# Kernel tuning notes

Measured on AMD Instinct MI355X. Metric: run time of the kernel, lower is better.

## Reference

```python
import jax, jax.numpy as jnp
import numpy as np
import math

N_ENT = 200000
N_USERS = 100000
N_FACTORS = 4
N_REL = 26
CH = 64
N_EDGES = 1000000
NNZ = 1000000
KG_HEADS = 2


def scatter_softmax(scores, seg, num_segments):
    # numerically-stable softmax over groups defined by seg (per-head softmax)
    m = jax.ops.segment_max(scores, seg, num_segments=num_segments)
    m = jnp.where(jnp.isfinite(m), m, 0.0)
    e = jnp.exp(scores - m[seg])
    d = jax.ops.segment_sum(e, seg, num_segments=num_segments)
    return e / d[seg]


def setup_inputs() -> dict:
    key = jax.random.key(0)
    ks = jax.random.split(key, 11)
    return {
        "entity_emb": jax.random.normal(ks[0], (N_ENT, CH), dtype=jnp.float32) * 0.1,
        "user_emb": jax.random.normal(ks[1], (N_USERS, CH), dtype=jnp.float32) * 0.1,
        "latent_emb": jax.random.normal(ks[2], (N_FACTORS, CH), dtype=jnp.float32) * 0.1,
        "edge_index": jax.random.randint(ks[3], (2, N_EDGES), 0, N_ENT),
        "edge_type": jax.random.randint(ks[4], (N_EDGES,), 1, N_REL),  # in [1, N_REL-1]
        "ui_rows": jax.random.randint(ks[5], (NNZ,), 0, N_USERS),
        "ui_cols": jax.random.randint(ks[6], (NNZ,), 0, N_ENT),
        "ui_vals": jax.random.uniform(ks[7], (NNZ,), dtype=jnp.float32),
        "weight": jax.random.normal(ks[8], (N_REL - 1, CH), dtype=jnp.float32) * 0.1,
        "disen_weight_att": jax.random.normal(ks[9], (N_FACTORS, N_REL - 1), dtype=jnp.float32) * 0.1,
        "kg_W_r": jax.random.normal(ks[10], (CH, CH), dtype=jnp.float32) * (1.0 / math.sqrt(CH)),
    }


def reference(entity_emb, user_emb, latent_emb, edge_index, edge_type,
              ui_rows, ui_cols, ui_vals, weight, disen_weight_att, kg_W_r):
    head, tail = edge_index[0], edge_index[1]
    d_k = CH // KG_HEADS

    # --- Invariant_Capture.relation_aware_att ---
    rel_emb = weight[edge_type - 1]            # [E, C] gather
    h_emb = entity_emb[head]                   # [E, C] gather
    q = (h_emb @ kg_W_r).reshape(-1, KG_HEADS, d_k)
    k = (rel_emb @ kg_W_r).reshape(-1, KG_HEADS, d_k)
    score_r = ((q * k).sum(-1) / math.sqrt(d_k)).mean(-1)   # [E]
    rel_attn = scatter_softmax(score_r, head, N_ENT)

    # --- Invariant_Capture.kg_inv_capture ---
    t_emb = entity_emb[tail]                   # [E, C] gather
    r_emb = rel_emb * rel_attn[:, None]
    # bmm(cat(h,r), cat(t,r)^T) == h.t + r.r per edge
    score_trip = (h_emb * t_emb).sum(-1) + (r_emb * r_emb).sum(-1)
    kg_mask = scatter_softmax(score_trip, head, N_ENT)       # invariant_mask [E]

    # --- Aggregator: KG scatter-mean with invariant mask ---
    neigh = t_emb * rel_emb * kg_mask[:, None]               # [E, C]
    sums = jax.ops.segment_sum(neigh, head, num_segments=N_ENT)
    cnt = jax.ops.segment_sum(jnp.ones((neigh.shape[0],), dtype=neigh.dtype), head, num_segments=N_ENT)
    entity_agg = sums / jnp.maximum(cnt, 1.0)[:, None]       # scatter_mean

    # --- Aggregator: user side ---
    score = jax.nn.softmax(user_emb @ latent_emb.T, axis=1)  # [U, F]
    user_agg = jax.ops.segment_sum(entity_emb[ui_cols] * ui_vals[:, None], ui_rows, num_segments=N_USERS)
    disen_weight = jax.nn.softmax(disen_weight_att, axis=-1) @ weight  # [F, C]
    # (expand(U,F,C) * score[:,:,None]).sum(1) == score @ disen_weight
    user_agg = user_agg * (score @ disen_weight) + user_agg

    return jnp.concatenate([entity_agg, user_agg], axis=0)   # [N_ENT+N_USERS, C]
```

## Files before the change

### kernel.cpp

```cpp
#include <hip/hip_runtime.h>
#include <math.h>

#define N_ENT 200000
#define N_USERS 100000
#define NKEY 300000
#define N_FACTORS 4
#define NREL1 25
#define CH 64
#define N_EDGES 1000000
#define NNZ 1000000
#define NREC 2000000
#define BSHIFT 11
#define BKEYS 2048
#define NBUCKET 147
#define TILE 2048
#define NBLK_FILL ((NREC + TILE - 1) / TILE)
#define CAP 32768
#define NCONVB ((N_ENT * 8 + 1023) / 1024)

#define SCORE_SCALE 0.08838834764831845f
#define INV_Q14 6.103888176768602e-05f

__device__ __forceinline__ float red8(float d) {
    d += __shfl_xor(d, 1);
    d += __shfl_xor(d, 2);
    d += __shfl_xor(d, 4);
    return d;
}
__device__ __forceinline__ float dot4(float4 a, float4 b) {
    return a.x * b.x + a.y * b.y + a.z * b.z + a.w * b.w;
}
__device__ __forceinline__ unsigned short f2bf(float f) {
    unsigned u = __float_as_uint(f);
    u += 0x7FFFu + ((u >> 16) & 1u);
    return (unsigned short)(u >> 16);
}
__device__ __forceinline__ float bf2f(unsigned short u) {
    return __uint_as_float(((unsigned)u) << 16);
}
__device__ __forceinline__ float4 bf4lo(uint4 t) {
    return make_float4(__uint_as_float(t.x << 16), __uint_as_float(t.x & 0xFFFF0000u),
                       __uint_as_float(t.y << 16), __uint_as_float(t.y & 0xFFFF0000u));
}
__device__ __forceinline__ float4 bf4hi(uint4 t) {
    return make_float4(__uint_as_float(t.z << 16), __uint_as_float(t.z & 0xFFFF0000u),
                       __uint_as_float(t.w << 16), __uint_as_float(t.w & 0xFFFF0000u));
}

__device__ __forceinline__
void precompute_dev(int tid, unsigned char* shmraw,
                    const float* __restrict__ W,
                    const float* __restrict__ weight,
                    const float* __restrict__ datt,
                    float* __restrict__ Mvec,
                    float* __restrict__ wnorm,
                    float* __restrict__ disen) {
    float* sW   = (float*)shmraw;
    float* sw   = sW + 4096;
    float* sWWt = sw + 1600;
    for (int i = tid; i < 64 * 64; i += 256) sW[i] = W[i];
    for (int i = tid; i < NREL1 * 64; i += 256) sw[i] = weight[i];
    __syncthreads();
    for (int e = tid; e < 64 * 64; e += 256) {
        int i = e >> 6, j = e & 63;
        float s = 0.f;
        for (int k = 0; k < 64; ++k) s += sW[i * 64 + k] * sW[j * 64 + k];
        sWWt[e] = s;
    }
    __syncthreads();
    for (int e = tid; e < NREL1 * 64; e += 256) {
        int r = e >> 6, i = e & 63;
        float s = 0.f;
        for (int j = 0; j < 64; ++j) s += sWWt[i * 64 + j] * sw[r * 64 + j];
        Mvec[e] = s;
    }
    for (int r = tid; r < NREL1; r += 256) {
        float s = 0.f;
        for (int j = 0; j < 64; ++j) { float v = sw[r * 64 + j]; s += v * v; }
        wnorm[r] = s;
    }
    for (int e = tid; e < N_FACTORS * 64; e += 256) {
        int f = e >> 6, c = e & 63;
        float m = -1e30f;
        for (int r = 0; r < NREL1; ++r) m = fmaxf(m, datt[f * NREL1 + r]);
        float ssum = 0.f, acc = 0.f;
        for (int r = 0; r < NREL1; ++r) {
            float p = expf(datt[f * NREL1 + r] - m);
            ssum += p;
            acc += p * sw[r * 64 + c];
        }
        disen[e] = acc / ssum;
    }
}

__global__ void binpre_k(const int* __restrict__ head, const int* __restrict__ tail,
                         const int* __restrict__ etype,
                         const int* __restrict__ rows, const int* __restrict__ cols,
                         const float* __restrict__ vals,
                         unsigned* __restrict__ gcur,
                         uint2* __restrict__ stg,
                         const float* __restrict__ W,
                         const float* __restrict__ weight,
                         const float* __restrict__ datt,
                         float* __restrict__ Mvec,
                         float* __restrict__ wnorm,
                         float* __restrict__ disen) {
    __shared__ __align__(16) unsigned char shmraw[39936];
    int tid = threadIdx.x;
    if (blockIdx.x >= NBLK_FILL) {
        precompute_dev(tid, shmraw, W, weight, datt, Mvec, wnorm, disen);
        return;
    }
    unsigned* hist  = (unsigned*)shmraw;
    unsigned* base  = hist + NBUCKET;
    unsigned* gbase = base + NBUCKET;
    unsigned* wsum  = gbase + NBUCKET;
    uint2*    lrec  = (uint2*)(shmraw + 2048);

    int tile0 = blockIdx.x * TILE;
    int tile_n = min(TILE, NREC - tile0);
    for (int b = tid; b < NBUCKET; b += 256) hist[b] = 0u;
    __syncthreads();
    unsigned key[8], pay[8], rank[8];
    for (int r = 0; r < 8; ++r) {
        int li = r * 256 + tid;
        key[r] = 0xFFFFFFFFu;
        if (li < tile_n) {
            int idx = tile0 + li;
            unsigned k, p;
            if (idx < N_EDGES) {
                k = (unsigned)head[idx];
                p = (unsigned)tail[idx] | ((unsigned)(etype[idx] - 1) << 18);
            } else {
                int j = idx - N_EDGES;
                k = (unsigned)(N_ENT + rows[j]);
                unsigned q = (unsigned)(vals[j] * 16383.f + 0.5f);
                p = (unsigned)cols[j] | (q << 18);
            }
            key[r] = k; pay[r] = p;
            rank[r] = atomicAdd(&hist[k >> BSHIFT], 1u);
        }
    }
    __syncthreads();
    unsigned h0 = (tid < NBUCKET) ? hist[tid] : 0u;
    unsigned v = h0;
    int lane = tid & 63, wid = tid >> 6;
    for (int o = 1; o < 64; o <<= 1) {
        unsigned t = __shfl_up(v, o);
        if (lane >= o) v += t;
    }
    if (lane == 63) wsum[wid] = v;
    __syncthreads();
    unsigned pre = 0;
    for (int w = 0; w < wid; ++w) pre += wsum[w];
    if (tid < NBUCKET) {
        base[tid] = pre + v - h0;
        gbase[tid] = (unsigned)tid * CAP + (h0 ? atomicAdd(&gcur[tid], h0) : 0u);
    }
    __syncthreads();
    for (int r = 0; r < 8; ++r) {
        if (key[r] != 0xFFFFFFFFu) {
            unsigned b = key[r] >> BSHIFT;
            lrec[base[b] + rank[r]] = make_uint2(key[r], pay[r]);
        }
    }
    __syncthreads();
    for (int i = tid; i < tile_n; i += 256) {
        uint2 rec = lrec[i];
        unsigned b = rec.x >> BSHIFT;
        unsigned dst = gbase[b] + ((unsigned)i - base[b]);
        if (dst < (b + 1u) * CAP) stg[dst] = rec;
    }
}

__device__ __forceinline__
void place_bucket_dev(int b, int tid, const uint2* __restrict__ stg,
                      const unsigned* __restrict__ gcur,
                      unsigned* __restrict__ offs, unsigned* __restrict__ csr,
                      unsigned* shm) {
    unsigned c = (tid < NBUCKET) ? gcur[tid] : 0u;
    if (c > CAP) c = CAP;
    if (tid < 256) shm[tid] = c;
    __syncthreads();
    for (int o = 1; o < 256; o <<= 1) {
        unsigned t = (tid >= o && tid < 256) ? shm[tid - o] : 0u;
        __syncthreads();
        if (tid < 256) shm[tid] += t;
        __syncthreads();
    }
    if (tid == 0) {
        unsigned cb = gcur[b]; if (cb > CAP) cb = CAP;
        shm[3073] = cb;
        shm[3072] = shm[b] - cb;
        if (b == NBUCKET - 1) offs[NKEY] = shm[NBUCKET - 1];
    }
    __syncthreads();
    unsigned n = shm[3073], gb = shm[3072];
    const uint2* seg = stg + (size_t)b * CAP;
    unsigned* cnt = shm;
    unsigned* sc  = shm + 2048;
    cnt[tid * 2] = 0u; cnt[tid * 2 + 1] = 0u;
    __syncthreads();
    for (unsigned i = tid; i < n; i += 1024) {
        unsigned kk = seg[i].x - ((unsigned)b << BSHIFT);
        atomicAdd(&cnt[kk], 1u);
    }
    __syncthreads();
    unsigned c0 = cnt[tid * 2], c1 = cnt[tid * 2 + 1];
    unsigned tsum = c0 + c1;
    sc[tid] = tsum; __syncthreads();
    for (int o = 1; o < 1024; o <<= 1) {
        unsigned t = (tid >= o) ? sc[tid - o] : 0u;
        __syncthreads();
        sc[tid] += t;
        __syncthreads();
    }
    unsigned e0 = sc[tid] - tsum;
    unsigned e1 = e0 + c0;
    int k0 = (b << BSHIFT) + tid * 2;
    if (k0 < NKEY)     offs[k0]     = gb + e0;
    if (k0 + 1 < NKEY) offs[k0 + 1] = gb + e1;
    cnt[tid * 2] = e0; cnt[tid * 2 + 1] = e1;
    __syncthreads();
    for (unsigned i = tid; i < n; i += 1024) {
        uint2 rec = seg[i];
        unsigned kk = rec.x - ((unsigned)b << BSHIFT);
        unsigned pos = atomicAdd(&cnt[kk], 1u);
        csr[gb + pos] = rec.y;
    }
}

__device__ __forceinline__
void convE_dev(int cb, int tid, const float* __restrict__ ent,
               const float* __restrict__ Mvec,
               uint4* __restrict__ entb, unsigned short* __restrict__ E16,
               unsigned* shm) {
    float4* sM = (float4*)shm;
    for (int i = tid; i < NREL1 * 16; i += 1024) sM[i] = ((const float4*)Mvec)[i];
    __syncthreads();
    int idx = cb * 1024 + tid;
    int h = idx >> 3;
    int sub = tid & 7;
    if (h >= N_ENT) return;
    const float4* e4 = (const float4*)ent;
    float4 a = e4[h * 16 + sub * 2], b4 = e4[h * 16 + sub * 2 + 1];
    uint4 o;
    o.x = (unsigned)f2bf(a.x)  | ((unsigned)f2bf(a.y)  << 16);
    o.y = (unsigned)f2bf(a.z)  | ((unsigned)f2bf(a.w)  << 16);
    o.z = (unsigned)f2bf(b4.x) | ((unsigned)f2bf(b4.y) << 16);
    o.w = (unsigned)f2bf(b4.z) | ((unsigned)f2bf(b4.w) << 16);
    entb[h * 8 + sub] = o;
    for (int r = 0; r < NREL1; ++r) {
        float d = dot4(a, sM[r * 16 + sub * 2]) + dot4(b4, sM[r * 16 + sub * 2 + 1]);
        d = red8(d);
        if (sub == (r & 7)) E16[h * NREL1 + r] = f2bf(__expf(d * SCORE_SCALE));
    }
}

__global__ void placeconv_k(const uint2* __restrict__ stg,
                            const unsigned* __restrict__ gcur,
                            unsigned* __restrict__ offs,
                            unsigned* __restrict__ csr,
                            const float* __restrict__ ent,
                            const float* __restrict__ Mvec,
                            uint4* __restrict__ entb,
                            unsigned short* __restrict__ E16) {
    __shared__ __align__(16) unsigned shm[3074];
    int b = blockIdx.x;
    if (b < NBUCKET)
        place_bucket_dev(b, threadIdx.x, stg, gcur, offs, csr, shm);
    else
        convE_dev(b - NBUCKET, threadIdx.x, ent, Mvec, entb, E16, shm);
}

__global__ void binplace3_k(const uint2* __restrict__ stg,
                            const unsigned* __restrict__ gcur,
                            unsigned* __restrict__ offs,
                            unsigned* __restrict__ csr) {
    __shared__ __align__(16) unsigned shm[3074];
    place_bucket_dev(blockIdx.x, threadIdx.x, stg, gcur, offs, csr, shm);
}

template<bool FAST>
__global__ void gather8_k(const float* __restrict__ ent,
                          const uint4* __restrict__ entb,
                          const unsigned short* __restrict__ E16,
                          const float* __restrict__ weight,
                          const float* __restrict__ Mvec,
                          const float* __restrict__ wnorm,
                          const float* __restrict__ uemb,
                          const float* __restrict__ lat,
                          const float* __restrict__ disen,
                          const unsigned* __restrict__ offs,
                          const unsigned* __restrict__ csr,
                          float* __restrict__ out) {
    int gid = blockIdx.x * 256 + threadIdx.x;
    int key = gid >> 3;
    int sub = threadIdx.x & 7;
    if (key >= NKEY) return;
    unsigned beg = offs[key], end = offs[key + 1];
    const float4* e4 = (const float4*)ent;
    const float4* w4 = (const float4*)weight;
    float4* o4 = (float4*)out;
    const float4 z = make_float4(0.f, 0.f, 0.f, 0.f);

    if (key < N_ENT) {
        int h = key;
        if (beg == end) {
            o4[h * 16 + sub * 2] = z;
            o4[h * 16 + sub * 2 + 1] = z;
            return;
        }
        float4 hv0, hv1;
        if (FAST) {
            uint4 hb = entb[h * 8 + sub];
            hv0 = bf4lo(hb); hv1 = bf4hi(hb);
        } else {
            hv0 = e4[h * 16 + sub * 2]; hv1 = e4[h * 16 + sub * 2 + 1];
        }
        float dr = 0.f;
        if (FAST) {
            for (unsigned i = beg + sub; i < end; i += 8)
                dr += bf2f(E16[h * NREL1 + (csr[i] >> 18)]);
            dr = red8(dr);
        } else {
            for (unsigned i = beg; i < end; ++i) {
                int r = csr[i] >> 18;
                float d = dot4(hv0, ((const float4*)Mvec)[r * 16 + sub * 2]) +
                          dot4(hv1, ((const float4*)Mvec)[r * 16 + sub * 2 + 1]);
                dr += __expf(red8(d) * SCORE_SCALE);
            }
        }
        float inv_dr = 1.0f / dr;
        float4 a0 = z, a1 = z;
        float dt = 0.f;
        unsigned i = beg;
        for (; i + 2 <= end; i += 2) {
            unsigned p0 = csr[i], p1 = csr[i + 1];
            int t0 = p0 & 0x3FFFF, r0 = p0 >> 18;
            int t1 = p1 & 0x3FFFF, r1 = p1 >> 18;
            float4 tv00, tv01, tv10, tv11;
            if (FAST) {
                uint4 tb0 = entb[t0 * 8 + sub];
                uint4 tb1 = entb[t1 * 8 + sub];
                tv00 = bf4lo(tb0); tv01 = bf4hi(tb0);
                tv10 = bf4lo(tb1); tv11 = bf4hi(tb1);
            } else {
                tv00 = e4[t0 * 16 + sub * 2]; tv01 = e4[t0 * 16 + sub * 2 + 1];
                tv10 = e4[t1 * 16 + sub * 2]; tv11 = e4[t1 * 16 + sub * 2 + 1];
            }
            float d0 = red8(dot4(hv0, tv00) + dot4(hv1, tv01));
            float d1 = red8(dot4(hv0, tv10) + dot4(hv1, tv11));
            float er0, er1;
            if (FAST) {
                er0 = bf2f(E16[h * NREL1 + r0]);
                er1 = bf2f(E16[h * NREL1 + r1]);
            } else {
                float q0 = dot4(hv0, ((const float4*)Mvec)[r0 * 16 + sub * 2]) +
                           dot4(hv1, ((const float4*)Mvec)[r0 * 16 + sub * 2 + 1]);
                float q1 = dot4(hv0, ((const float4*)Mvec)[r1 * 16 + sub * 2]) +
                           dot4(hv1, ((const float4*)Mvec)[r1 * 16 + sub * 2 + 1]);
                er0 = __expf(red8(q0) * SCORE_SCALE);
                er1 = __expf(red8(q1) * SCORE_SCALE);
            }
            float ra0 = er0 * inv_dr, ra1 = er1 * inv_dr;
            float et0 = __expf(d0 + ra0 * ra0 * wnorm[r0]);
            float et1 = __expf(d1 + ra1 * ra1 * wnorm[r1]);
            dt += et0 + et1;
            float4 wv;
            wv = w4[r0 * 16 + sub * 2];
            a0.x += et0 * tv00.x * wv.x; a0.y += et0 * tv00.y * wv.y;
            a0.z += et0 * tv00.z * wv.z; a0.w += et0 * tv00.w * wv.w;
            wv = w4[r0 * 16 + sub * 2 + 1];
            a1.x += et0 * tv01.x * wv.x; a1.y += et0 * tv01.y * wv.y;
            a1.z += et0 * tv01.z * wv.z; a1.w += et0 * tv01.w * wv.w;
            wv = w4[r1 * 16 + sub * 2];
            a0.x += et1 * tv10.x * wv.x; a0.y += et1 * tv10.y * wv.y;
            a0.z += et1 * tv10.z * wv.z; a0.w += et1 * tv10.w * wv.w;
            wv = w4[r1 * 16 + sub * 2 + 1];
            a1.x += et1 * tv11.x * wv.x; a1.y += et1 * tv11.y * wv.y;
            a1.z += et1 * tv11.z * wv.z; a1.w += et1 * tv11.w * wv.w;
        }
        if (i < end) {
            unsigned p = csr[i];
            int t = p & 0x3FFFF, r = p >> 18;
            float4 tv0, tv1;
            if (FAST) {
                uint4 tb = entb[t * 8 + sub];
                tv0 = bf4lo(tb); tv1 = bf4hi(tb);
            } else {
                tv0 = e4[t * 16 + sub * 2]; tv1 = e4[t * 16 + sub * 2 + 1];
            }
            float d = red8(dot4(hv0, tv0) + dot4(hv1, tv1));
            float er;
            if (FAST) {
                er = bf2f(E16[h * NREL1 + r]);
            } else {
                float q = dot4(hv0, ((const float4*)Mvec)[r * 16 + sub * 2]) +
                          dot4(hv1, ((const float4*)Mvec)[r * 16 + sub * 2 + 1]);
                er = __expf(red8(q) * SCORE_SCALE);
            }
            float ra = er * inv_dr;
            float et = __expf(d + ra * ra * wnorm[r]);
            dt += et;
            float4 wv;
            wv = w4[r * 16 + sub * 2];
            a0.x += et * tv0.x * wv.x; a0.y += et * tv0.y * wv.y;
            a0.z += et * tv0.z * wv.z; a0.w += et * tv0.w * wv.w;
            wv = w4[r * 16 + sub * 2 + 1];
            a1.x += et * tv1.x * wv.x; a1.y += et * tv1.y * wv.y;
            a1.z += et * tv1.z * wv.z; a1.w += et * tv1.w * wv.w;
        }
        float inv = 1.0f / (dt * (float)(end - beg));
        a0.x *= inv; a0.y *= inv; a0.z *= inv; a0.w *= inv;
        a1.x *= inv; a1.y *= inv; a1.z *= inv; a1.w *= inv;
        o4[h * 16 + sub * 2] = a0;
        o4[h * 16 + sub * 2 + 1] = a1;
    } else {
        int u = key - N_ENT;
        float4 a0 = z, a1 = z;
        unsigned i = beg;
        for (; i + 2 <= end; i += 2) {
            unsigned p0 = csr[i], p1 = csr[i + 1];
            int c0 = p0 & 0x3FFFF, c1 = p1 & 0x3FFFF;
            float v0 = (float)(p0 >> 18) * INV_Q14;
            float v1 = (float)(p1 >> 18) * INV_Q14;
            float4 tv00, tv01, tv10, tv11;
            if (FAST) {
                uint4 tb0 = entb[c0 * 8 + sub];
                uint4 tb1 = entb[c1 * 8 + sub];
                tv00 = bf4lo(tb0); tv01 = bf4hi(tb0);
                tv10 = bf4lo(tb1); tv11 = bf4hi(tb1);
            } else {
                tv00 = e4[c0 * 16 + sub * 2]; tv01 = e4[c0 * 16 + sub * 2 + 1];
                tv10 = e4[c1 * 16 + sub * 2]; tv11 = e4[c1 * 16 + sub * 2 + 1];
            }
            a0.x += v0 * tv00.x + v1 * tv10.x; a0.y += v0 * tv00.y + v1 * tv10.y;
            a0.z += v0 * tv00.z + v1 * tv10.z; a0.w += v0 * tv00.w + v1 * tv10.w;
            a1.x += v0 * tv01.x + v1 * tv11.x; a1.y += v0 * tv01.y + v1 * tv11.y;
            a1.z += v0 * tv01.z + v1 * tv11.z; a1.w += v0 * tv01.w + v1 * tv11.w;
        }
        if (i < end) {
            unsigned p = csr[i];
            int c = p & 0x3FFFF;
            float v = (float)(p >> 18) * INV_Q14;
            float4 tv0, tv1;
            if (FAST) {
                uint4 tb = entb[c * 8 + sub];
                tv0 = bf4lo(tb); tv1 = bf4hi(tb);
            } else {
                tv0 = e4[c * 16 + sub * 2]; tv1 = e4[c * 16 + sub * 2 + 1];
            }
            a0.x += v * tv0.x; a0.y += v * tv0.y; a0.z += v * tv0.z; a0.w += v * tv0.w;
            a1.x += v * tv1.x; a1.y += v * tv1.y; a1.z += v * tv1.z; a1.w += v * tv1.w;
        }
        float4 uv0 = ((const float4*)uemb)[u * 16 + sub * 2];
        float4 uv1 = ((const float4*)uemb)[u * 16 + sub * 2 + 1];
        float d[N_FACTORS];
        for (int f = 0; f < N_FACTORS; ++f) {
            float t = dot4(uv0, ((const float4*)lat)[f * 16 + sub * 2]) +
                      dot4(uv1, ((const float4*)lat)[f * 16 + sub * 2 + 1]);
            d[f] = red8(t);
        }
        float m = fmaxf(fmaxf(d[0], d[1]), fmaxf(d[2], d[3]));
        float s = 0.f, p_[N_FACTORS];
        for (int f = 0; f < N_FACTORS; ++f) { p_[f] = __expf(d[f] - m); s += p_[f]; }
        float invs = 1.0f / s;
        float4 g0 = z, g1 = z;
        for (int f = 0; f < N_FACTORS; ++f) {
            float w = p_[f] * invs;
            float4 dv = ((const float4*)disen)[f * 16 + sub * 2];
            g0.x += w * dv.x; g0.y += w * dv.y; g0.z += w * dv.z; g0.w += w * dv.w;
            dv = ((const float4*)disen)[f * 16 + sub * 2 + 1];
            g1.x += w * dv.x; g1.y += w * dv.y; g1.z += w * dv.z; g1.w += w * dv.w;
        }
        a0.x *= (1.0f + g0.x); a0.y *= (1.0f + g0.y);
        a0.z *= (1.0f + g0.z); a0.w *= (1.0f + g0.w);
        a1.x *= (1.0f + g1.x); a1.y *= (1.0f + g1.y);
        a1.z *= (1.0f + g1.z); a1.w *= (1.0f + g1.w);
        o4[key * 16 + sub * 2] = a0;
        o4[key * 16 + sub * 2 + 1] = a1;
    }
}

extern "C" void kernel_launch(void* const* d_in, const int* in_sizes, int n_in,
                              void* d_out, int out_size, void* d_ws, size_t ws_size,
                              hipStream_t stream) {
    (void)in_sizes; (void)n_in; (void)out_size;
    const float* ent    = (const float*)d_in[0];
    const float* uemb   = (const float*)d_in[1];
    const float* lat    = (const float*)d_in[2];
    const int*   eidx   = (const int*)d_in[3];
    const int*   etype  = (const int*)d_in[4];
    const int*   urows  = (const int*)d_in[5];
    const int*   ucols  = (const int*)d_in[6];
    const float* uvals  = (const float*)d_in[7];
    const float* weight = (const float*)d_in[8];
    const float* datt   = (const float*)d_in[9];
    const float* W      = (const float*)d_in[10];

    const int* head = eidx;
    const int* tail = eidx + N_EDGES;
    float* out = (float*)d_out;

    uint2* stg = (uint2*)d_out;

    unsigned* gcur  = (unsigned*)d_ws;
    unsigned* offs  = gcur + 256;
    float*    Mvec  = (float*)(offs + NKEY + 2);
    float*    wnorm = Mvec + NREL1 * 64;
    float*    disen = wnorm + 32;
    unsigned* csr   = (unsigned*)(disen + N_FACTORS * 64);
    unsigned* entw  = csr + NREC;
    uint4*    entb  = (uint4*)entw;
    unsigned short* E16 = (unsigned short*)(entw + (size_t)N_ENT * 32);

    size_t base_words = 256 + (NKEY + 2) + 1888 + (size_t)NREC;
    size_t tbl_words  = (size_t)N_ENT * 32 + ((size_t)N_ENT * NREL1 + 1) / 2;
    size_t need_fast  = (base_words + tbl_words) * 4;
    size_t need_min   = base_words * 4;
    size_t need_out   = (size_t)NBUCKET * CAP * 8;
    bool fast = (ws_size >= need_fast) &&
                ((size_t)out_size * 4 >= need_out);
    if (ws_size < need_min || (size_t)out_size * 4 < need_out) return;

    const int BLK = 256;

    hipMemsetAsync(gcur, 0, 256 * sizeof(unsigned), stream);
    binpre_k<<<NBLK_FILL + 1, BLK, 0, stream>>>(
        head, tail, etype, urows, ucols, uvals, gcur, stg,
        W, weight, datt, Mvec, wnorm, disen);

    if (fast) {
        placeconv_k<<<NBUCKET + NCONVB, 1024, 0, stream>>>(
            stg, gcur, offs, csr, ent, Mvec, entb, E16);
    } else {
        binplace3_k<<<NBUCKET, 1024, 0, stream>>>(stg, gcur, offs, csr);
    }

    int gridG = (NKEY * 8 + BLK - 1) / BLK;
    if (fast) {
        gather8_k<true><<<gridG, BLK, 0, stream>>>(
            ent, entb, E16, weight, Mvec, wnorm,
            uemb, lat, disen, offs, csr, out);
    } else {
        gather8_k<false><<<gridG, BLK, 0, stream>>>(
            ent, entb, E16, weight, Mvec, wnorm,
            uemb, lat, disen, offs, csr, out);
    }
}
```

Before: 198.1 us.

## Gather KG entity rows from an FP8 table and split binning histograms per wave

After: 196.1 us. No clear change (-1.0%).

```diff
diff --git a/kernel.cpp b/kernel.cpp
--- a/kernel.cpp
+++ b/kernel.cpp
@@ -21,6 +21,8 @@
 #define SCORE_SCALE 0.08838834764831845f
 #define INV_Q14 6.103888176768602e-05f
 
+typedef __attribute__((ext_vector_type(2))) float floatx2;
+
 __device__ __forceinline__ float red8(float d) {
     d += __shfl_xor(d, 1);
     d += __shfl_xor(d, 2);
@@ -45,6 +47,21 @@
 __device__ __forceinline__ float4 bf4hi(uint4 t) {
     return make_float4(__uint_as_float(t.z << 16), __uint_as_float(t.z & 0xFFFF0000u),
                        __uint_as_float(t.w << 16), __uint_as_float(t.w & 0xFFFF0000u));
+}
+__device__ __forceinline__ void fp8x8_dec(uint2 v, float4& lo, float4& hi) {
+    floatx2 a = __builtin_amdgcn_cvt_pk_f32_fp8((int)v.x, false);
+    floatx2 b = __builtin_amdgcn_cvt_pk_f32_fp8((int)v.x, true);
+    floatx2 c = __builtin_amdgcn_cvt_pk_f32_fp8((int)v.y, false);
+    floatx2 d = __builtin_amdgcn_cvt_pk_f32_fp8((int)v.y, true);
+    lo = make_float4(a[0], a[1], b[0], b[1]);
+    hi = make_float4(c[0], c[1], d[0], d[1]);
+}
+__device__ __forceinline__ uint2 fp8x8_enc(float4 lo, float4 hi) {
+    int l = __builtin_amdgcn_cvt_pk_fp8_f32(lo.x, lo.y, 0, false);
+    l = __builtin_amdgcn_cvt_pk_fp8_f32(lo.z, lo.w, l, true);
+    int h = __builtin_amdgcn_cvt_pk_fp8_f32(hi.x, hi.y, 0, false);
+    h = __builtin_amdgcn_cvt_pk_fp8_f32(hi.z, hi.w, h, true);
+    return make_uint2((unsigned)l, (unsigned)h);
 }
 
 __device__ __forceinline__
@@ -112,15 +129,16 @@
         return;
     }
     unsigned* hist  = (unsigned*)shmraw;
-    unsigned* base  = hist + NBUCKET;
-    unsigned* gbase = base + NBUCKET;
-    unsigned* wsum  = gbase + NBUCKET;
-    uint2*    lrec  = (uint2*)(shmraw + 2048);
+    unsigned* base  = hist + 640;
+    unsigned* gbase = base + 160;
+    unsigned* wsum  = gbase + 160;
+    uint2*    lrec  = (uint2*)(shmraw + 4096);
 
     int tile0 = blockIdx.x * TILE;
     int tile_n = min(TILE, NREC - tile0);
-    for (int b = tid; b < NBUCKET; b += 256) hist[b] = 0u;
-    __syncthreads();
+    for (int i = tid; i < 640; i += 256) hist[i] = 0u;
+    __syncthreads();
+    int wid = tid >> 6;
     unsigned key[8], pay[8], rank[8];
     for (int r = 0; r < 8; ++r) {
         int li = r * 256 + tid;
@@ -138,13 +156,22 @@
                 p = (unsigned)cols[j] | (q << 18);
             }
             key[r] = k; pay[r] = p;
-            rank[r] = atomicAdd(&hist[k >> BSHIFT], 1u);
-        }
-    }
-    __syncthreads();
-    unsigned h0 = (tid < NBUCKET) ? hist[tid] : 0u;
-    unsigned v = h0;
-    int lane = tid & 63, wid = tid >> 6;
+            rank[r] = atomicAdd(&hist[wid * 160 + (k >> BSHIFT)], 1u);
+        }
+    }
+    __syncthreads();
+    unsigned tot = 0;
+    if (tid < NBUCKET) {
+        unsigned h0 = hist[tid], h1 = hist[160 + tid];
+        unsigned h2 = hist[320 + tid], h3 = hist[480 + tid];
+        tot = h0 + h1 + h2 + h3;
+        hist[tid] = 0u;
+        hist[160 + tid] = h0;
+        hist[320 + tid] = h0 + h1;
+        hist[480 + tid] = h0 + h1 + h2;
+    }
+    unsigned v = tot;
+    int lane = tid & 63;
     for (int o = 1; o < 64; o <<= 1) {
         unsigned t = __shfl_up(v, o);
         if (lane >= o) v += t;
@@ -154,14 +181,14 @@
     unsigned pre = 0;
     for (int w = 0; w < wid; ++w) pre += wsum[w];
     if (tid < NBUCKET) {
-        base[tid] = pre + v - h0;
-        gbase[tid] = (unsigned)tid * CAP + (h0 ? atomicAdd(&gcur[tid], h0) : 0u);
+        base[tid] = pre + v - tot;
+        gbase[tid] = (unsigned)tid * CAP + (tot ? atomicAdd(&gcur[tid], tot) : 0u);
     }
     __syncthreads();
     for (int r = 0; r < 8; ++r) {
         if (key[r] != 0xFFFFFFFFu) {
             unsigned b = key[r] >> BSHIFT;
-            lrec[base[b] + rank[r]] = make_uint2(key[r], pay[r]);
+            lrec[base[b] + hist[wid * 160 + b] + rank[r]] = make_uint2(key[r], pay[r]);
         }
     }
     __syncthreads();
@@ -230,11 +257,12 @@
     }
 }
 
+template<bool W8>
 __device__ __forceinline__
 void convE_dev(int cb, int tid, const float* __restrict__ ent,
                const float* __restrict__ Mvec,
                uint4* __restrict__ entb, unsigned short* __restrict__ E16,
-               unsigned* shm) {
+               uint2* __restrict__ ent8, unsigned* shm) {
     float4* sM = (float4*)shm;
     for (int i = tid; i < NREL1 * 16; i += 1024) sM[i] = ((const float4*)Mvec)[i];
     __syncthreads();
@@ -250,6 +278,7 @@
     o.z = (unsigned)f2bf(b4.x) | ((unsigned)f2bf(b4.y) << 16);
     o.w = (unsigned)f2bf(b4.z) | ((unsigned)f2bf(b4.w) << 16);
     entb[h * 8 + sub] = o;
+    if (W8) ent8[h * 8 + sub] = fp8x8_enc(a, b4);
     for (int r = 0; r < NREL1; ++r) {
         float d = dot4(a, sM[r * 16 + sub * 2]) + dot4(b4, sM[r * 16 + sub * 2 + 1]);
         d = red8(d);
@@ -257,6 +286,7 @@
     }
 }
 
+template<bool W8>
 __global__ void placeconv_k(const uint2* __restrict__ stg,
                             const unsigned* __restrict__ gcur,
                             unsigned* __restrict__ offs,
@@ -264,13 +294,14 @@
                             const float* __restrict__ ent,
                             const float* __restrict__ Mvec,
                             uint4* __restrict__ entb,
-                            unsigned short* __restrict__ E16) {
+                            unsigned short* __restrict__ E16,
+                            uint2* __restrict__ ent8) {
     __shared__ __align__(16) unsigned shm[3074];
     int b = blockIdx.x;
     if (b < NBUCKET)
         place_bucket_dev(b, threadIdx.x, stg, gcur, offs, csr, shm);
     else
-        convE_dev(b - NBUCKET, threadIdx.x, ent, Mvec, entb, E16, shm);
+        convE_dev<W8>(b - NBUCKET, threadIdx.x, ent, Mvec, entb, E16, ent8, shm);
 }
 
 __global__ void binplace3_k(const uint2* __restrict__ stg,
@@ -281,9 +312,24 @@
     place_bucket_dev(blockIdx.x, threadIdx.x, stg, gcur, offs, csr, shm);
 }
 
-template<bool FAST>
+template<int MODE>
+__device__ __forceinline__
+void ent_row(const uint4* entb, const uint2* ent8, const float4* e4,
+             int t, int sub, float4& lo, float4& hi) {
+    if (MODE == 2) {
+        fp8x8_dec(ent8[t * 8 + sub], lo, hi);
+    } else if (MODE == 1) {
+        uint4 tb = entb[t * 8 + sub];
+        lo = bf4lo(tb); hi = bf4hi(tb);
+    } else {
+        lo = e4[t * 16 + sub * 2]; hi = e4[t * 16 + sub * 2 + 1];
+    }
+}
+
+template<int MODE>
 __global__ void gather8_k(const float* __restrict__ ent,
                           const uint4* __restrict__ entb,
+                          const uint2* __restrict__ ent8,
                           const unsigned short* __restrict__ E16,
                           const float* __restrict__ weight,
                           const float* __restrict__ Mvec,
@@ -312,14 +358,9 @@
             return;
         }
         float4 hv0, hv1;
-        if (FAST) {
-            uint4 hb = entb[h * 8 + sub];
-            hv0 = bf4lo(hb); hv1 = bf4hi(hb);
-        } else {
-            hv0 = e4[h * 16 + sub * 2]; hv1 = e4[h * 16 + sub * 2 + 1];
-        }
+        ent_row<MODE>(entb, ent8, e4, h, sub, hv0, hv1);
         float dr = 0.f;
-        if (FAST) {
+        if (MODE > 0) {
             for (unsigned i = beg + sub; i < end; i += 8)
                 dr += bf2f(E16[h * NREL1 + (csr[i] >> 18)]);
             dr = red8(dr);
@@ -340,19 +381,12 @@
             int t0 = p0 & 0x3FFFF, r0 = p0 >> 18;
             int t1 = p1 & 0x3FFFF, r1 = p1 >> 18;
             float4 tv00, tv01, tv10, tv11;
-            if (FAST) {
-                uint4 tb0 = entb[t0 * 8 + sub];
-                uint4 tb1 = entb[t1 * 8 + sub];
-                tv00 = bf4lo(tb0); tv01 = bf4hi(tb0);
-                tv10 = bf4lo(tb1); tv11 = bf4hi(tb1);
-            } else {
-                tv00 = e4[t0 * 16 + sub * 2]; tv01 = e4[t0 * 16 + sub * 2 + 1];
-                tv10 = e4[t1 * 16 + sub * 2]; tv11 = e4[t1 * 16 + sub * 2 + 1];
-            }
+            ent_row<MODE>(entb, ent8, e4, t0, sub, tv00, tv01);
+            ent_row<MODE>(entb, ent8, e4, t1, sub, tv10, tv11);
             float d0 = red8(dot4(hv0, tv00) + dot4(hv1, tv01));
             float d1 = red8(dot4(hv0, tv10) + dot4(hv1, tv11));
             float er0, er1;
-            if (FAST) {
+            if (MODE > 0) {
                 er0 = bf2f(E16[h * NREL1 + r0]);
                 er1 = bf2f(E16[h * NREL1 + r1]);
             } else {
@@ -385,15 +419,10 @@
             unsigned p = csr[i];
             int t = p & 0x3FFFF, r = p >> 18;
             float4 tv0, tv1;
-            if (FAST) {
-                uint4 tb = entb[t * 8 + sub];
-                tv0 = bf4lo(tb); tv1 = bf4hi(tb);
-            } else {
-                tv0 = e4[t * 16 + sub * 2]; tv1 = e4[t * 16 + sub * 2 + 1];
-            }
+            ent_row<MODE>(entb, ent8, e4, t, sub, tv0, tv1);
             float d = red8(dot4(hv0, tv0) + dot4(hv1, tv1));
             float er;
-            if (FAST) {
+            if (MODE > 0) {
                 er = bf2f(E16[h * NREL1 + r]);
             } else {
                 float q = dot4(hv0, ((const float4*)Mvec)[r * 16 + sub * 2]) +
@@ -426,15 +455,8 @@
             float v0 = (float)(p0 >> 18) * INV_Q14;
             float v1 = (float)(p1 >> 18) * INV_Q14;
             float4 tv00, tv01, tv10, tv11;
-            if (FAST) {
-                uint4 tb0 = entb[c0 * 8 + sub];
-                uint4 tb1 = entb[c1 * 8 + sub];
-                tv00 = bf4lo(tb0); tv01 = bf4hi(tb0);
-                tv10 = bf4lo(tb1); tv11 = bf4hi(tb1);
-            } else {
-                tv00 = e4[c0 * 16 + sub * 2]; tv01 = e4[c0 * 16 + sub * 2 + 1];
-                tv10 = e4[c1 * 16 + sub * 2]; tv11 = e4[c1 * 16 + sub * 2 + 1];
-            }
+            ent_row<(MODE > 0 ? 1 : 0)>(entb, ent8, e4, c0, sub, tv00, tv01);
+            ent_row<(MODE > 0 ? 1 : 0)>(entb, ent8, e4, c1, sub, tv10, tv11);
             a0.x += v0 * tv00.x + v1 * tv10.x; a0.y += v0 * tv00.y + v1 * tv10.y;
             a0.z += v0 * tv00.z + v1 * tv10.z; a0.w += v0 * tv00.w + v1 * tv10.w;
             a1.x += v0 * tv01.x + v1 * tv11.x; a1.y += v0 * tv01.y + v1 * tv11.y;
@@ -445,12 +467,7 @@
             int c = p & 0x3FFFF;
             float v = (float)(p >> 18) * INV_Q14;
             float4 tv0, tv1;
-            if (FAST) {
-                uint4 tb = entb[c * 8 + sub];
-                tv0 = bf4lo(tb); tv1 = bf4hi(tb);
-            } else {
-                tv0 = e4[c * 16 + sub * 2]; tv1 = e4[c * 16 + sub * 2 + 1];
-            }
+            ent_row<(MODE > 0 ? 1 : 0)>(entb, ent8, e4, c, sub, tv0, tv1);
             a0.x += v * tv0.x; a0.y += v * tv0.y; a0.z += v * tv0.z; a0.w += v * tv0.w;
             a1.x += v * tv1.x; a1.y += v * tv1.y; a1.z += v * tv1.z; a1.w += v * tv1.w;
         }
@@ -514,15 +531,15 @@
     unsigned* entw  = csr + NREC;
     uint4*    entb  = (uint4*)entw;
     unsigned short* E16 = (unsigned short*)(entw + (size_t)N_ENT * 32);
+    uint2*    ent8  = (uint2*)(entw + (size_t)N_ENT * 32 +
+                               ((size_t)N_ENT * NREL1 + 1) / 2);
 
     size_t base_words = 256 + (NKEY + 2) + 1888 + (size_t)NREC;
-    size_t tbl_words  = (size_t)N_ENT * 32 + ((size_t)N_ENT * NREL1 + 1) / 2;
-    size_t need_fast  = (base_words + tbl_words) * 4;
-    size_t need_min   = base_words * 4;
-    size_t need_out   = (size_t)NBUCKET * CAP * 8;
-    bool fast = (ws_size >= need_fast) &&
-                ((size_t)out_size * 4 >= need_out);
-    if (ws_size < need_min || (size_t)out_size * 4 < need_out) return;
+    size_t need1 = (base_words + 8900000ull) * 4;
+    size_t need2 = (base_words + 12100000ull) * 4;
+    size_t need_out = (size_t)NBUCKET * CAP * 8;
+    int mode = (ws_size >= need2) ? 2 : (ws_size >= need1) ? 1 : 0;
+    if (ws_size < base_words * 4 || (size_t)out_size * 4 < need_out) return;
 
     const int BLK = 256;
 
@@ -531,21 +548,28 @@
         head, tail, etype, urows, ucols, uvals, gcur, stg,
         W, weight, datt, Mvec, wnorm, disen);
 
-    if (fast) {
-        placeconv_k<<<NBUCKET + NCONVB, 1024, 0, stream>>>(
-            stg, gcur, offs, csr, ent, Mvec, entb, E16);
+    if (mode == 2) {
+        placeconv_k<true><<<NBUCKET + NCONVB, 1024, 0, stream>>>(
+            stg, gcur, offs, csr, ent, Mvec, entb, E16, ent8);
+    } else if (mode == 1) {
+        placeconv_k<false><<<NBUCKET + NCONVB, 1024, 0, stream>>>(
+            stg, gcur, offs, csr, ent, Mvec, entb, E16, ent8);
     } else {
         binplace3_k<<<NBUCKET, 1024, 0, stream>>>(stg, gcur, offs, csr);
     }
 
     int gridG = (NKEY * 8 + BLK - 1) / BLK;
-    if (fast) {
-        gather8_k<true><<<gridG, BLK, 0, stream>>>(
-            ent, entb, E16, weight, Mvec, wnorm,
+    if (mode == 2) {
+        gather8_k<2><<<gridG, BLK, 0, stream>>>(
+            ent, entb, ent8, E16, weight, Mvec, wnorm,
+            uemb, lat, disen, offs, csr, out);
+    } else if (mode == 1) {
+        gather8_k<1><<<gridG, BLK, 0, stream>>>(
+            ent, entb, ent8, E16, weight, Mvec, wnorm,
             uemb, lat, disen, offs, csr, out);
     } else {
-        gather8_k<false><<<gridG, BLK, 0, stream>>>(
-            ent, entb, E16, weight, Mvec, wnorm,
+        gather8_k<0><<<gridG, BLK, 0, stream>>>(
+            ent, entb, ent8, E16, weight, Mvec, wnorm,
             uemb, lat, disen, offs, csr, out);
     }
 }
```
